# Performance work log

Measured on AMD Instinct MI355X. Metric: run time of the kernel, lower is better.

## Reference

```python
import jax, jax.numpy as jnp
import numpy as np

B, N, D, H = 4, 1024, 256, 8  # batch, seq, in_dim(=per-head qkv_dim), n_heads


def setup_inputs() -> dict:
    key = jax.random.key(0)
    k1, k2, k3 = jax.random.split(key, 3)
    x = jax.random.normal(k1, (B, N, D), dtype=jnp.float32)
    Wqkv = jax.random.normal(k2, (D, 3 * D * H), dtype=jnp.float32) * 0.02
    bqkv = jnp.zeros((3 * D * H,), dtype=jnp.float32)
    W0 = jax.random.normal(k3, (D * H, D), dtype=jnp.float32) * 0.02
    b0 = jnp.zeros((D,), dtype=jnp.float32)
    return {"x": x, "Wqkv": Wqkv, "bqkv": bqkv, "W0": W0, "b0": b0}


def reference(x, Wqkv, bqkv, W0, b0):
    b, n, d = x.shape
    h = Wqkv.shape[1] // (3 * d)
    qkv = x @ Wqkv + bqkv                      # [b, n, 3*d*h]
    # Faithful to torch: raw row-major reinterpretation of the buffer.
    q, k, v = jnp.reshape(qkv, (3, b, n, d, h))
    score = jnp.einsum('bnqh,btqh->bnth', q, k) * (d ** -0.5)  # [b, n, n, h]
    attn = jax.nn.softmax(score, axis=1)       # softmax over query axis (dim=1), as in source
    # einsum 'bnnh,bnqh->bnqh' = diagonal of attn times v (faithful to source)
    av = jnp.einsum('bnnh,bnqh->bnqh', attn, v)  # [b, n, d, h]
    out = av.reshape(b, n, d * h) @ W0 + b0    # [b, n, d]
    return out
```

## Files before the change

### kernel.cpp

```cpp
#include <hip/hip_runtime.h>


#define SEGSZ 8388608

typedef short v8s __attribute__((ext_vector_type(8)));
typedef float v4f __attribute__((ext_vector_type(4)));

__device__ __forceinline__ ushort f2bf(float v) {
  union { float f; unsigned u; } x; x.f = v;
  const unsigned r = x.u + 0x7fff + ((x.u >> 16) & 1);
  return (ushort)(r >> 16);
}
__device__ __forceinline__ float bf2f(ushort v) {
  union { unsigned u; float f; } x; x.u = ((unsigned)v) << 16;
  return x.f;
}

#define GLOAD_LDS16(g, l)                                            \
  __builtin_amdgcn_global_load_lds(                                  \
      (const __attribute__((address_space(1))) void*)(g),            \
      (__attribute__((address_space(3))) void*)(l), 16, 0, 0)

__global__ __launch_bounds__(256) void prep(
    const float* __restrict__ X, const float* __restrict__ Wqkv,
    const float* __restrict__ W0, ushort* __restrict__ xb,
    ushort* __restrict__ whT, ushort* __restrict__ w0T) {
  __shared__ float T[64][65];
  const int tid = threadIdx.x;
  int bid = blockIdx.x;

  if (bid < 1024) {
    const size_t i = ((size_t)bid * 256 + tid) * 4;
    const float4 v = *(const float4*)&X[i];
    ushort4 hv = {f2bf(v.x), f2bf(v.y), f2bf(v.z), f2bf(v.w)};
    *(ushort4*)&xb[i] = hv;
    return;
  }
  bid -= 1024;
  if (bid < 384) {
    const int n0 = (bid % 96) * 64;
    const int k0 = (bid / 96) * 64;
    {
      const int row = tid >> 2;
      const int c0 = (tid & 3) * 16;
#pragma unroll
      for (int j = 0; j < 16; j += 4) {
        const float4 v = *(const float4*)&Wqkv[(size_t)(k0 + row) * 6144 + n0 + c0 + j];
        T[row][c0 + j + 0] = v.x; T[row][c0 + j + 1] = v.y;
        T[row][c0 + j + 2] = v.z; T[row][c0 + j + 3] = v.w;
      }
    }
    __syncthreads();
    {
      const int nn = tid >> 2;
      const int kk0 = (tid & 3) * 16;
      const int n = n0 + nn;
      const int seg = n >> 11, h = n & 7, d = (n & 2047) >> 3;
      const int p = seg * 2048 + h * 256 + d;
      ushort hv[16];
#pragma unroll
      for (int j = 0; j < 16; ++j) hv[j] = f2bf(T[kk0 + j][nn]);
      const size_t base = (size_t)p * 256 + k0 + kk0;
#pragma unroll
      for (int j = 0; j < 16; j += 8) *(v8s*)&whT[base + j] = *(v8s*)&hv[j];
    }
    return;
  }
  bid -= 384;
  {
    const int e0 = (bid & 3) * 64;
    const int k0 = (bid >> 2) * 64;
    {
      const int row = tid >> 2;
      const int c0 = (tid & 3) * 16;
#pragma unroll
      for (int j = 0; j < 16; j += 4) {
        const float4 v = *(const float4*)&W0[(size_t)(k0 + row) * 256 + e0 + c0 + j];
        T[row][c0 + j + 0] = v.x; T[row][c0 + j + 1] = v.y;
        T[row][c0 + j + 2] = v.z; T[row][c0 + j + 3] = v.w;
      }
    }
    __syncthreads();
    {
      const int ee = tid >> 2;
      const int kk0 = (tid & 3) * 16;
#pragma unroll
      for (int j = 0; j < 16; ++j) {
        const int k = k0 + kk0 + j;
        const int d = k >> 3, h = k & 7;
        w0T[(size_t)(e0 + ee) * 2048 + h * 256 + d] = f2bf(T[kk0 + j][ee]);
      }
    }
  }
}

__global__ __launch_bounds__(256) void qkv_mfma(
    const ushort* __restrict__ xb, const ushort* __restrict__ whT,
    const float* __restrict__ bias, ushort* __restrict__ qkvb) {
  __shared__ ushort As[128 * 32];
  __shared__ ushort Bh[128 * 32];
  const int tid = threadIdx.x;
  const int wave = tid >> 6, lane = tid & 63;
  const int quad = lane >> 4, l15 = lane & 15;
  const int c0 = blockIdx.x * 128;
  const int r0 = blockIdx.y * 128;
  const int wr = (wave >> 1) * 64;
  const int wc = (wave & 1) * 64;

  v4f acc[4][4] = {};

  for (int d0 = 0; d0 < 256; d0 += 32) {
#pragma unroll
    for (int half = 0; half < 2; ++half) {
      const int rr = wave * 32 + half * 16;
      const int row = rr + (lane >> 2);
      const int gcol = d0 + (lane & 3) * 8;
      GLOAD_LDS16(xb + (size_t)(r0 + row) * 256 + gcol, &As[rr * 32]);
      GLOAD_LDS16(whT + (size_t)(c0 + row) * 256 + gcol, &Bh[rr * 32]);
    }
    __syncthreads();

    v8s aF[4], bF[4];
#pragma unroll
    for (int i = 0; i < 4; ++i) {
      aF[i] = *(const v8s*)&As[(wr + i * 16 + l15) * 32 + quad * 8];
      bF[i] = *(const v8s*)&Bh[(wc + i * 16 + l15) * 32 + quad * 8];
    }
#pragma unroll
    for (int ri = 0; ri < 4; ++ri)
#pragma unroll
      for (int ci = 0; ci < 4; ++ci)
        acc[ri][ci] = __builtin_amdgcn_mfma_f32_16x16x32_bf16(
            aF[ri], bF[ci], acc[ri][ci], 0, 0, 0);
    __syncthreads();
  }

#pragma unroll
  for (int ci = 0; ci < 4; ++ci) {
    const int c = c0 + wc + ci * 16 + l15;
    const int cseg = c >> 11;
    const int h = (c & 2047) >> 8;
    const int d = c & 255;
    const float bv = bias[cseg * 2048 + d * 8 + h];
#pragma unroll
    for (int ri = 0; ri < 4; ++ri)
#pragma unroll
      for (int rg = 0; rg < 4; ++rg) {
        const int r = r0 + wr + ri * 16 + quad * 4 + rg;
        const int g = r * 3 + cseg;
        const int seg = g >> 12;
        const int tok = g & 4095;
        float val = acc[ri][ci][rg] + bv;
        if (seg == 0) val *= 0.0625f;
        qkvb[(size_t)seg * SEGSZ + (size_t)tok * 2048 + h * 256 + d] = f2bf(val);
      }
  }
}

__global__ __launch_bounds__(256) void mid_fused(
    const ushort* __restrict__ qkvb, const ushort* __restrict__ w0T,
    float* __restrict__ pl, float* __restrict__ sd_ws,
    ushort* __restrict__ partial) {
  __shared__ ushort S1[128 * 32];
  __shared__ ushort S2[128 * 32];
  __shared__ float redL[2][2][64];

  const int tid = threadIdx.x;
  const int wave = tid >> 6, lane = tid & 63;
  const int quad = lane >> 4, l15 = lane & 15;
  const int wr = (wave >> 1) * 64;
  const int wc = (wave & 1) * 64;
  const int id = blockIdx.x;

  v4f acc[4][4] = {};

  if (id < 2048) {
    const int bh = (id >> 9) * 8 + (id & 7);
    const int tile = (id >> 3) & 63;
    const int tt0 = (tile >> 3) * 128;
    const int nn0 = (tile & 7) * 128;
    const int b = bh >> 3, h = bh & 7;
    const ushort* Qg = qkvb + (size_t)b * 1024 * 2048 + h * 256;
    const ushort* Kg = Qg + SEGSZ;

    for (int d0 = 0; d0 < 256; d0 += 32) {
#pragma unroll
      for (int half = 0; half < 2; ++half) {
        const int rr = wave * 32 + half * 16;
        const int row = rr + (lane >> 2);
        const int gcol = d0 + (lane & 3) * 8;
        GLOAD_LDS16(Qg + (size_t)(nn0 + row) * 2048 + gcol, &S1[rr * 32]);
        GLOAD_LDS16(Kg + (size_t)(tt0 + row) * 2048 + gcol, &S2[rr * 32]);
      }
      __syncthreads();

      v8s aF[4], bF[4];
#pragma unroll
      for (int i = 0; i < 4; ++i) {
        aF[i] = *(const v8s*)&S1[(wr + i * 16 + l15) * 32 + quad * 8];
        bF[i] = *(const v8s*)&S2[(wc + i * 16 + l15) * 32 + quad * 8];
      }
#pragma unroll
      for (int ri = 0; ri < 4; ++ri)
#pragma unroll
        for (int ci = 0; ci < 4; ++ci)
          acc[ri][ci] = __builtin_amdgcn_mfma_f32_16x16x32_bf16(
              aF[ri], bF[ci], acc[ri][ci], 0, 0, 0);
      __syncthreads();
    }

    float lsum[4];
#pragma unroll
    for (int ci = 0; ci < 4; ++ci) {
      float s = 0.f;
#pragma unroll
      for (int ri = 0; ri < 4; ++ri)
#pragma unroll
        for (int rg = 0; rg < 4; ++rg) s += __expf(acc[ri][ci][rg]);
      s += __shfl_xor(s, 16, 64);
      s += __shfl_xor(s, 32, 64);
      lsum[ci] = s;
    }
    if (quad == 0) {
#pragma unroll
      for (int ci = 0; ci < 4; ++ci)
        redL[wave & 1][wave >> 1][ci * 16 + l15] = lsum[ci];
    }
    __syncthreads();
    if ((wave >> 1) == 0 && quad == 0) {
#pragma unroll
      for (int ci = 0; ci < 4; ++ci) {
        const int t = tt0 + (wave & 1) * 64 + ci * 16 + l15;
        const float l = lsum[ci] + redL[wave & 1][1][ci * 16 + l15];
        pl[((size_t)bh * 1024 + t) * 8 + (tile & 7)] = l;
      }
    }

    if (tt0 == nn0 && (wave == 0 || wave == 3) && quad == (l15 >> 2)) {
#pragma unroll
      for (int ri = 0; ri < 4; ++ri) {
        const int t = tt0 + (wave & 1) * 64 + ri * 16 + l15;
        sd_ws[(size_t)bh * 1024 + t] = acc[ri][ri][l15 & 3];
      }
    }
  } else {
    const int j = id - 2048;
    const int e0 = (j & 1) * 128;
    const int tok0 = ((j >> 1) & 31) * 128;
    const int h = j >> 6;
    const int kbase = h * 256;
    const ushort* vb = qkvb + 2 * (size_t)SEGSZ;

    for (int d0 = 0; d0 < 256; d0 += 32) {
#pragma unroll
      for (int half = 0; half < 2; ++half) {
        const int rr = wave * 32 + half * 16;
        const int row = rr + (lane >> 2);
        const int gcol = kbase + d0 + (lane & 3) * 8;
        GLOAD_LDS16(vb + (size_t)(tok0 + row) * 2048 + gcol, &S1[rr * 32]);
        GLOAD_LDS16(w0T + (size_t)(e0 + row) * 2048 + gcol, &S2[rr * 32]);
      }
      __syncthreads();

      v8s aF[4], bF[4];
#pragma unroll
      for (int i = 0; i < 4; ++i) {
        aF[i] = *(const v8s*)&S1[(wr + i * 16 + l15) * 32 + quad * 8];
        bF[i] = *(const v8s*)&S2[(wc + i * 16 + l15) * 32 + quad * 8];
      }
#pragma unroll
      for (int ri = 0; ri < 4; ++ri)
#pragma unroll
        for (int ci = 0; ci < 4; ++ci)
          acc[ri][ci] = __builtin_amdgcn_mfma_f32_16x16x32_bf16(
              aF[ri], bF[ci], acc[ri][ci], 0, 0, 0);
      __syncthreads();
    }

#pragma unroll
    for (int ri = 0; ri < 4; ++ri)
#pragma unroll
      for (int rg = 0; rg < 4; ++rg) {
        const int lrow = wr + ri * 16 + quad * 4 + rg;
        const int tok = tok0 + lrow;
#pragma unroll
        for (int ci = 0; ci < 4; ++ci) {
          const int e = e0 + wc + ci * 16 + l15;
          partial[(size_t)h * 1048576 + (size_t)tok * 256 + e] =
              f2bf(acc[ri][ci][rg]);
        }
      }
  }
}

__global__ __launch_bounds__(256) void av_atomic(
    const ushort* __restrict__ vb, const ushort* __restrict__ w0T,
    const float* __restrict__ pl, const float* __restrict__ sd,
    float* __restrict__ out) {
  __shared__ ushort As[128 * 32];
  __shared__ ushort Bs[128 * 32];
  __shared__ float diagS[128];
  const int tid = threadIdx.x;
  const int wave = tid >> 6, lane = tid & 63;
  const int quad = lane >> 4, l15 = lane & 15;
  const int e0 = blockIdx.x * 128;
  const int tok0 = blockIdx.y * 128;
  const int h = blockIdx.z;
  const int kbase = h * 256;
  const int wr = (wave >> 1) * 64;
  const int wc = (wave & 1) * 64;

  if (tid < 128) {
    const int bh = (tok0 >> 10) * 8 + h;
    const int t = (tok0 & 1023) + tid;
    const size_t base = ((size_t)bh * 1024 + t) * 8;
    float l = 0.f;
#pragma unroll
    for (int c = 0; c < 8; ++c) l += pl[base + c];
    diagS[tid] = __expf(sd[(size_t)bh * 1024 + t]) / l;
  }

  v4f acc[4][4] = {};

  for (int d0 = 0; d0 < 256; d0 += 32) {
#pragma unroll
    for (int half = 0; half < 2; ++half) {
      const int rr = wave * 32 + half * 16;
      const int row = rr + (lane >> 2);
      const int gcol = kbase + d0 + (lane & 3) * 8;
      GLOAD_LDS16(vb + (size_t)(tok0 + row) * 2048 + gcol, &As[rr * 32]);
      GLOAD_LDS16(w0T + (size_t)(e0 + row) * 2048 + gcol, &Bs[rr * 32]);
    }
    __syncthreads();

    v8s aF[4], bF[4];
#pragma unroll
    for (int i = 0; i < 4; ++i) {
      aF[i] = *(const v8s*)&As[(wr + i * 16 + l15) * 32 + quad * 8];
      bF[i] = *(const v8s*)&Bs[(wc + i * 16 + l15) * 32 + quad * 8];
    }
#pragma unroll
    for (int ri = 0; ri < 4; ++ri)
#pragma unroll
      for (int ci = 0; ci < 4; ++ci)
        acc[ri][ci] =
            __builtin_amdgcn_mfma_f32_16x16x32_bf16(aF[ri], bF[ci], acc[ri][ci], 0, 0, 0);
    __syncthreads();
  }

#pragma unroll
  for (int ri = 0; ri < 4; ++ri)
#pragma unroll
    for (int rg = 0; rg < 4; ++rg) {
      const int lrow = wr + ri * 16 + quad * 4 + rg;
      const int tok = tok0 + lrow;
      const float dg = diagS[lrow];
#pragma unroll
      for (int ci = 0; ci < 4; ++ci) {
        const int e = e0 + wc + ci * 16 + l15;
        atomicAdd(&out[(size_t)tok * 256 + e], acc[ri][ci][rg] * dg);
      }
    }
}

__global__ void init_out(const float* __restrict__ b0, float* __restrict__ out) {
  const int i = blockIdx.x * 256 + threadIdx.x;
  const int e0 = (i & 63) << 2;
  *(float4*)&out[(size_t)i * 4] = *(const float4*)&b0[e0];
}

__global__ void reduce_out(const ushort* __restrict__ partial,
                           const float* __restrict__ pl,
                           const float* __restrict__ sd,
                           const float* __restrict__ b0, float* __restrict__ out) {
  __shared__ float dgS[32];
  const int i = blockIdx.x * 256 + threadIdx.x;
  const int tbase = blockIdx.x * 4;
  if (threadIdx.x < 32) {
    const int tl = threadIdx.x >> 3, h = threadIdx.x & 7;
    const int tok = tbase + tl;
    const int bh = (tok >> 10) * 8 + h;
    const int t = tok & 1023;
    const size_t base = ((size_t)bh * 1024 + t) * 8;
    float l = 0.f;
#pragma unroll
    for (int c = 0; c < 8; ++c) l += pl[base + c];
    dgS[threadIdx.x] = __expf(sd[(size_t)bh * 1024 + t]) / l;
  }
  __syncthreads();
  const int tl = threadIdx.x >> 6;
  const int e0 = (i & 63) << 2;
  float4 a = *(const float4*)&b0[e0];
#pragma unroll
  for (int h = 0; h < 8; ++h) {
    const float dg = dgS[tl * 8 + h];
    const ushort4 p = *(const ushort4*)&partial[(size_t)h * 1048576 + (size_t)i * 4];
    a.x += dg * bf2f(p.x); a.y += dg * bf2f(p.y);
    a.z += dg * bf2f(p.z); a.w += dg * bf2f(p.w);
  }
  *(float4*)&out[(size_t)i * 4] = a;
}

extern "C" void kernel_launch(void* const* d_in, const int* in_sizes, int n_in,
                              void* d_out, int out_size, void* d_ws, size_t ws_size,
                              hipStream_t stream) {
  const float* x    = (const float*)d_in[0];
  const float* Wqkv = (const float*)d_in[1];
  const float* bqkv = (const float*)d_in[2];
  const float* W0   = (const float*)d_in[3];
  const float* b0   = (const float*)d_in[4];
  float* out = (float*)d_out;

  float*  pl   = (float*)d_ws;
  float*  sd   = pl + 262144;
  ushort* qkvb = (ushort*)(sd + 32768);
  ushort* xb   = qkvb + 3 * (size_t)SEGSZ;
  ushort* whT  = xb + 1048576;
  ushort* w0T  = whT + 1572864;
  ushort* partial = w0T + 524288;

  ushort* vb = qkvb + 2 * (size_t)SEGSZ;

  const size_t need_base =
      (size_t)(262144 + 32768) * 4 + (size_t)SEGSZ * 3 * 2 +
      (size_t)(1048576 + 1572864 + 524288) * 2;
  const bool full = ws_size >= need_base + (size_t)8 * 1048576 * 2;

  prep<<<1536, 256, 0, stream>>>(x, Wqkv, W0, xb, whT, w0T);
  qkv_mfma<<<dim3(48, 32), 256, 0, stream>>>(xb, whT, bqkv, qkvb);
  if (full) {
    mid_fused<<<2560, 256, 0, stream>>>(qkvb, w0T, pl, sd, partial);
    reduce_out<<<1024, 256, 0, stream>>>(partial, pl, sd, b0, out);
  } else {
    scores_fallback:
    mid_fused<<<2048, 256, 0, stream>>>(qkvb, w0T, pl, sd, nullptr);
    init_out<<<1024, 256, 0, stream>>>(b0, out);
    av_atomic<<<dim3(2, 32, 8), 256, 0, stream>>>(vb, w0T, pl, sd, out);
  }
}
```

Baseline: 135.2 us.

## Use 256x256 double-buffered 8-wave GEMM tiles for QKV and mid kernels

Replaces the 128x128, 4-wave, single-buffered MFMA GEMMs with a shared 256x256, 8-wave routine. It double-buffers K-tiles of 64 in LDS with an XOR swizzle, and interleaves async global-to-LDS loads with MFMA phases using explicit vmcnt waits, barriers and setprio. The goal is more operand reuse per tile, hidden load latency and fewer LDS bank conflicts. Costs are larger LDS use (128KB per block), fewer blocks in the grid, and a partial-sum layout for pl that shrinks from 8 to 4 slots per token.

```diff
diff --git a/kernel.cpp b/kernel.cpp
--- a/kernel.cpp
+++ b/kernel.cpp
@@ -20,6 +20,10 @@
   __builtin_amdgcn_global_load_lds(                                  \
       (const __attribute__((address_space(1))) void*)(g),            \
       (__attribute__((address_space(3))) void*)(l), 16, 0, 0)
+
+#define SBAR()   asm volatile("s_barrier" ::: "memory")
+#define VMCNT4() asm volatile("s_waitcnt vmcnt(4)" ::: "memory")
+#define VMCNT0() asm volatile("s_waitcnt vmcnt(0)" ::: "memory")
 
 __global__ __launch_bounds__(256) void prep(
     const float* __restrict__ X, const float* __restrict__ Wqkv,
@@ -94,202 +98,219 @@
   }
 }
 
-__global__ __launch_bounds__(256) void qkv_mfma(
+template <int STRIDE>
+__device__ __forceinline__ void gemm256_8ph(
+    const ushort* __restrict__ gA, const ushort* __restrict__ gB,
+    ushort (&AS)[2][16384], ushort (&BS)[2][16384],
+    v4f (&acc)[2][2][4][2]) {
+  const int tid = threadIdx.x;
+  const int wave = tid >> 6, lane = tid & 63;
+  const int wm = wave >> 2, wn = wave & 3;
+  const int quad = lane >> 4, l15 = lane & 15;
+  const int srow = wave * 8 + (lane >> 3);
+  const int scol = ((lane & 7) << 3) ^ (((lane >> 5) & 1) << 4);
+  const int cq = (quad * 8) ^ (((l15 >> 2) & 1) << 4);
+
+  auto stage = [&](int op, int buf, int half, int kt) {
+#pragma unroll
+    for (int j = 0; j < 2; ++j) {
+      const size_t grow =
+          (size_t)(half * 128 + j * 64 + srow) * STRIDE + kt * 64 + scol;
+      ushort* lb = op ? &BS[buf][half * 8192 + j * 4096 + wave * 512]
+                      : &AS[buf][half * 8192 + j * 4096 + wave * 512];
+      GLOAD_LDS16((op ? gB : gA) + grow, lb);
+    }
+  };
+
+  stage(0, 0, 0, 0); stage(0, 0, 1, 0); stage(1, 0, 0, 0); stage(1, 0, 1, 0);
+  stage(0, 1, 0, 1); stage(1, 1, 0, 1);
+  VMCNT4();
+  SBAR();
+
+  for (int it = 0; it < 2; ++it) {
+    const int t0 = it * 2;
+#pragma unroll
+    for (int p = 0; p < 8; ++p) {
+      const int kb = p >> 2;
+      const int qr = (p >> 1) & 1, qc = p & 1;
+      v8s af[4][2], bfr[2][2];
+#pragma unroll
+      for (int ri = 0; ri < 4; ++ri) {
+        const int r = qr * 128 + wm * 64 + ri * 16 + l15;
+#pragma unroll
+        for (int ks = 0; ks < 2; ++ks)
+          af[ri][ks] = *(const v8s*)&AS[kb][r * 64 + ks * 32 + cq];
+      }
+#pragma unroll
+      for (int ci = 0; ci < 2; ++ci) {
+        const int r = qc * 128 + wn * 32 + ci * 16 + l15;
+#pragma unroll
+        for (int ks = 0; ks < 2; ++ks)
+          bfr[ci][ks] = *(const v8s*)&BS[kb][r * 64 + ks * 32 + cq];
+      }
+      {
+        const int st = t0 + 1 + ((p + 2) >> 2);
+        if (st < 4) stage(p & 1, st & 1, 1 - ((p >> 1) & 1), st);
+      }
+      SBAR();
+      __builtin_amdgcn_s_setprio(1);
+#pragma unroll
+      for (int ri = 0; ri < 4; ++ri)
+#pragma unroll
+        for (int ci = 0; ci < 2; ++ci)
+#pragma unroll
+          for (int ks = 0; ks < 2; ++ks)
+            acc[qr][qc][ri][ci] = __builtin_amdgcn_mfma_f32_16x16x32_bf16(
+                af[ri][ks], bfr[ci][ks], acc[qr][qc][ri][ci], 0, 0, 0);
+      __builtin_amdgcn_s_setprio(0);
+      if (p == 3 || p == 7) { if (it == 0) VMCNT4(); else VMCNT0(); }
+      SBAR();
+    }
+  }
+}
+
+__global__ __launch_bounds__(512, 2) void qkv8(
     const ushort* __restrict__ xb, const ushort* __restrict__ whT,
     const float* __restrict__ bias, ushort* __restrict__ qkvb) {
-  __shared__ ushort As[128 * 32];
-  __shared__ ushort Bh[128 * 32];
+  __shared__ ushort AS[2][16384];
+  __shared__ ushort BS[2][16384];
   const int tid = threadIdx.x;
   const int wave = tid >> 6, lane = tid & 63;
+  const int wm = wave >> 2, wn = wave & 3;
   const int quad = lane >> 4, l15 = lane & 15;
-  const int c0 = blockIdx.x * 128;
-  const int r0 = blockIdx.y * 128;
-  const int wr = (wave >> 1) * 64;
-  const int wc = (wave & 1) * 64;
-
-  v4f acc[4][4] = {};
-
-  for (int d0 = 0; d0 < 256; d0 += 32) {
-#pragma unroll
-    for (int half = 0; half < 2; ++half) {
-      const int rr = wave * 32 + half * 16;
-      const int row = rr + (lane >> 2);
-      const int gcol = d0 + (lane & 3) * 8;
-      GLOAD_LDS16(xb + (size_t)(r0 + row) * 256 + gcol, &As[rr * 32]);
-      GLOAD_LDS16(whT + (size_t)(c0 + row) * 256 + gcol, &Bh[rr * 32]);
-    }
-    __syncthreads();
-
-    v8s aF[4], bF[4];
-#pragma unroll
-    for (int i = 0; i < 4; ++i) {
-      aF[i] = *(const v8s*)&As[(wr + i * 16 + l15) * 32 + quad * 8];
-      bF[i] = *(const v8s*)&Bh[(wc + i * 16 + l15) * 32 + quad * 8];
-    }
-#pragma unroll
-    for (int ri = 0; ri < 4; ++ri)
-#pragma unroll
-      for (int ci = 0; ci < 4; ++ci)
-        acc[ri][ci] = __builtin_amdgcn_mfma_f32_16x16x32_bf16(
-            aF[ri], bF[ci], acc[ri][ci], 0, 0, 0);
-    __syncthreads();
-  }
-
-#pragma unroll
-  for (int ci = 0; ci < 4; ++ci) {
-    const int c = c0 + wc + ci * 16 + l15;
-    const int cseg = c >> 11;
-    const int h = (c & 2047) >> 8;
-    const int d = c & 255;
-    const float bv = bias[cseg * 2048 + d * 8 + h];
-#pragma unroll
-    for (int ri = 0; ri < 4; ++ri)
-#pragma unroll
-      for (int rg = 0; rg < 4; ++rg) {
-        const int r = r0 + wr + ri * 16 + quad * 4 + rg;
-        const int g = r * 3 + cseg;
-        const int seg = g >> 12;
-        const int tok = g & 4095;
-        float val = acc[ri][ci][rg] + bv;
-        if (seg == 0) val *= 0.0625f;
-        qkvb[(size_t)seg * SEGSZ + (size_t)tok * 2048 + h * 256 + d] = f2bf(val);
-      }
-  }
-}
-
-__global__ __launch_bounds__(256) void mid_fused(
+  const int c0 = blockIdx.x * 256;
+  const int r0 = blockIdx.y * 256;
+
+  v4f acc[2][2][4][2] = {};
+  gemm256_8ph<256>(xb + (size_t)r0 * 256, whT + (size_t)c0 * 256, AS, BS, acc);
+
+#pragma unroll
+  for (int qc2 = 0; qc2 < 2; ++qc2)
+#pragma unroll
+    for (int ci = 0; ci < 2; ++ci) {
+      const int cc = c0 + qc2 * 128 + wn * 32 + ci * 16 + l15;
+      const int cseg = cc >> 11;
+      const int hh = (cc & 2047) >> 8;
+      const int d = cc & 255;
+      const float bv = bias[cseg * 2048 + d * 8 + hh];
+#pragma unroll
+      for (int qr = 0; qr < 2; ++qr)
+#pragma unroll
+        for (int ri = 0; ri < 4; ++ri)
+#pragma unroll
+          for (int rg = 0; rg < 4; ++rg) {
+            const int r = r0 + qr * 128 + wm * 64 + ri * 16 + quad * 4 + rg;
+            const int g = r * 3 + cseg;
+            const int seg = g >> 12;
+            const int tok = g & 4095;
+            float val = acc[qr][qc2][ri][ci][rg] + bv;
+            if (seg == 0) val *= 0.0625f;
+            qkvb[(size_t)seg * SEGSZ + (size_t)tok * 2048 + hh * 256 + d] = f2bf(val);
+          }
+    }
+}
+
+__global__ __launch_bounds__(512, 2) void mid8(
     const ushort* __restrict__ qkvb, const ushort* __restrict__ w0T,
     float* __restrict__ pl, float* __restrict__ sd_ws,
     ushort* __restrict__ partial) {
-  __shared__ ushort S1[128 * 32];
-  __shared__ ushort S2[128 * 32];
-  __shared__ float redL[2][2][64];
-
+  __shared__ ushort AS[2][16384];
+  __shared__ ushort BS[2][16384];
+  __shared__ float redL[2][4][64];
   const int tid = threadIdx.x;
   const int wave = tid >> 6, lane = tid & 63;
+  const int wm = wave >> 2, wn = wave & 3;
   const int quad = lane >> 4, l15 = lane & 15;
-  const int wr = (wave >> 1) * 64;
-  const int wc = (wave & 1) * 64;
   const int id = blockIdx.x;
 
-  v4f acc[4][4] = {};
-
-  if (id < 2048) {
-    const int bh = (id >> 9) * 8 + (id & 7);
-    const int tile = (id >> 3) & 63;
-    const int tt0 = (tile >> 3) * 128;
-    const int nn0 = (tile & 7) * 128;
+  v4f acc[2][2][4][2] = {};
+
+  if (id < 512) {
+    const int c = id & 7, inner = id >> 3;
+    const int bh = (inner >> 4) * 8 + c;
+    const int tile = inner & 15;
+    const int tt0 = (tile >> 2) * 256;
+    const int nn0 = (tile & 3) * 256;
     const int b = bh >> 3, h = bh & 7;
-    const ushort* Qg = qkvb + (size_t)b * 1024 * 2048 + h * 256;
-    const ushort* Kg = Qg + SEGSZ;
-
-    for (int d0 = 0; d0 < 256; d0 += 32) {
-#pragma unroll
-      for (int half = 0; half < 2; ++half) {
-        const int rr = wave * 32 + half * 16;
-        const int row = rr + (lane >> 2);
-        const int gcol = d0 + (lane & 3) * 8;
-        GLOAD_LDS16(Qg + (size_t)(nn0 + row) * 2048 + gcol, &S1[rr * 32]);
-        GLOAD_LDS16(Kg + (size_t)(tt0 + row) * 2048 + gcol, &S2[rr * 32]);
-      }
-      __syncthreads();
-
-      v8s aF[4], bF[4];
-#pragma unroll
-      for (int i = 0; i < 4; ++i) {
-        aF[i] = *(const v8s*)&S1[(wr + i * 16 + l15) * 32 + quad * 8];
-        bF[i] = *(const v8s*)&S2[(wc + i * 16 + l15) * 32 + quad * 8];
-      }
+    const ushort* Qg = qkvb + (size_t)b * 2097152 + h * 256 + (size_t)nn0 * 2048;
+    const ushort* Kg = qkvb + SEGSZ + (size_t)b * 2097152 + h * 256 + (size_t)tt0 * 2048;
+    gemm256_8ph<2048>(Qg, Kg, AS, BS, acc);
+
+    float lsum[2][2];
+#pragma unroll
+    for (int qc2 = 0; qc2 < 2; ++qc2)
+#pragma unroll
+      for (int ci = 0; ci < 2; ++ci) {
+        float s = 0.f;
+#pragma unroll
+        for (int qr = 0; qr < 2; ++qr)
+#pragma unroll
+          for (int ri = 0; ri < 4; ++ri)
+#pragma unroll
+            for (int rg = 0; rg < 4; ++rg)
+              s += __expf(acc[qr][qc2][ri][ci][rg]);
+        s += __shfl_xor(s, 16, 64);
+        s += __shfl_xor(s, 32, 64);
+        lsum[qc2][ci] = s;
+      }
+    if (quad == 0) {
+#pragma unroll
+      for (int qc2 = 0; qc2 < 2; ++qc2)
+#pragma unroll
+        for (int ci = 0; ci < 2; ++ci)
+          redL[wm][wn][(qc2 * 2 + ci) * 16 + l15] = lsum[qc2][ci];
+    }
+    __syncthreads();
+    if (wm == 0 && quad == 0) {
+#pragma unroll
+      for (int qc2 = 0; qc2 < 2; ++qc2)
+#pragma unroll
+        for (int ci = 0; ci < 2; ++ci) {
+          const int t = tt0 + qc2 * 128 + wn * 32 + ci * 16 + l15;
+          const float l = lsum[qc2][ci] + redL[1][wn][(qc2 * 2 + ci) * 16 + l15];
+          pl[((size_t)bh * 1024 + t) * 4 + (nn0 >> 8)] = l;
+        }
+    }
+
+    if (tt0 == nn0) {
+#pragma unroll
+      for (int qr = 0; qr < 2; ++qr)
+#pragma unroll
+        for (int ci = 0; ci < 2; ++ci)
+#pragma unroll
+          for (int ri = 0; ri < 4; ++ri)
+#pragma unroll
+            for (int rg = 0; rg < 4; ++rg)
+              if (wn * 2 + ci - wm * 4 == ri && (l15 >> 2) == quad &&
+                  (l15 & 3) == rg) {
+                const int t = tt0 + qr * 128 + wm * 64 + ri * 16 + l15;
+                sd_ws[(size_t)bh * 1024 + t] = acc[qr][qr][ri][ci][rg];
+              }
+    }
+  } else {
+    const int j = id - 512;
+    const int h = j >> 4;
+    const int tok0 = (j & 15) * 256;
+    const ushort* Ag = qkvb + 2 * (size_t)SEGSZ + (size_t)tok0 * 2048 + h * 256;
+    const ushort* Bg = w0T + h * 256;
+    gemm256_8ph<2048>(Ag, Bg, AS, BS, acc);
+
+#pragma unroll
+    for (int qr = 0; qr < 2; ++qr)
 #pragma unroll
       for (int ri = 0; ri < 4; ++ri)
 #pragma unroll
-        for (int ci = 0; ci < 4; ++ci)
-          acc[ri][ci] = __builtin_amdgcn_mfma_f32_16x16x32_bf16(
-              aF[ri], bF[ci], acc[ri][ci], 0, 0, 0);
-      __syncthreads();
-    }
-
-    float lsum[4];
-#pragma unroll
-    for (int ci = 0; ci < 4; ++ci) {
-      float s = 0.f;
-#pragma unroll
-      for (int ri = 0; ri < 4; ++ri)
-#pragma unroll
-        for (int rg = 0; rg < 4; ++rg) s += __expf(acc[ri][ci][rg]);
-      s += __shfl_xor(s, 16, 64);
-      s += __shfl_xor(s, 32, 64);
-      lsum[ci] = s;
-    }
-    if (quad == 0) {
-#pragma unroll
-      for (int ci = 0; ci < 4; ++ci)
-        redL[wave & 1][wave >> 1][ci * 16 + l15] = lsum[ci];
-    }
-    __syncthreads();
-    if ((wave >> 1) == 0 && quad == 0) {
-#pragma unroll
-      for (int ci = 0; ci < 4; ++ci) {
-        const int t = tt0 + (wave & 1) * 64 + ci * 16 + l15;
-        const float l = lsum[ci] + redL[wave & 1][1][ci * 16 + l15];
-        pl[((size_t)bh * 1024 + t) * 8 + (tile & 7)] = l;
-      }
-    }
-
-    if (tt0 == nn0 && (wave == 0 || wave == 3) && quad == (l15 >> 2)) {
-#pragma unroll
-      for (int ri = 0; ri < 4; ++ri) {
-        const int t = tt0 + (wave & 1) * 64 + ri * 16 + l15;
-        sd_ws[(size_t)bh * 1024 + t] = acc[ri][ri][l15 & 3];
-      }
-    }
-  } else {
-    const int j = id - 2048;
-    const int e0 = (j & 1) * 128;
-    const int tok0 = ((j >> 1) & 31) * 128;
-    const int h = j >> 6;
-    const int kbase = h * 256;
-    const ushort* vb = qkvb + 2 * (size_t)SEGSZ;
-
-    for (int d0 = 0; d0 < 256; d0 += 32) {
-#pragma unroll
-      for (int half = 0; half < 2; ++half) {
-        const int rr = wave * 32 + half * 16;
-        const int row = rr + (lane >> 2);
-        const int gcol = kbase + d0 + (lane & 3) * 8;
-        GLOAD_LDS16(vb + (size_t)(tok0 + row) * 2048 + gcol, &S1[rr * 32]);
-        GLOAD_LDS16(w0T + (size_t)(e0 + row) * 2048 + gcol, &S2[rr * 32]);
-      }
-      __syncthreads();
-
-      v8s aF[4], bF[4];
-#pragma unroll
-      for (int i = 0; i < 4; ++i) {
-        aF[i] = *(const v8s*)&S1[(wr + i * 16 + l15) * 32 + quad * 8];
-        bF[i] = *(const v8s*)&S2[(wc + i * 16 + l15) * 32 + quad * 8];
-      }
-#pragma unroll
-      for (int ri = 0; ri < 4; ++ri)
-#pragma unroll
-        for (int ci = 0; ci < 4; ++ci)
-          acc[ri][ci] = __builtin_amdgcn_mfma_f32_16x16x32_bf16(
-              aF[ri], bF[ci], acc[ri][ci], 0, 0, 0);
-      __syncthreads();
-    }
-
-#pragma unroll
-    for (int ri = 0; ri < 4; ++ri)
-#pragma unroll
-      for (int rg = 0; rg < 4; ++rg) {
-        const int lrow = wr + ri * 16 + quad * 4 + rg;
-        const int tok = tok0 + lrow;
-#pragma unroll
-        for (int ci = 0; ci < 4; ++ci) {
-          const int e = e0 + wc + ci * 16 + l15;
-          partial[(size_t)h * 1048576 + (size_t)tok * 256 + e] =
-              f2bf(acc[ri][ci][rg]);
+        for (int rg = 0; rg < 4; ++rg) {
+          const int tok = tok0 + qr * 128 + wm * 64 + ri * 16 + quad * 4 + rg;
+#pragma unroll
+          for (int qc2 = 0; qc2 < 2; ++qc2)
+#pragma unroll
+            for (int ci = 0; ci < 2; ++ci) {
+              const int e = qc2 * 128 + wn * 32 + ci * 16 + l15;
+              partial[(size_t)h * 1048576 + (size_t)tok * 256 + e] =
+                  f2bf(acc[qr][qc2][ri][ci][rg]);
+            }
         }
-      }
   }
 }
 
@@ -313,10 +334,10 @@
   if (tid < 128) {
     const int bh = (tok0 >> 10) * 8 + h;
     const int t = (tok0 & 1023) + tid;
-    const size_t base = ((size_t)bh * 1024 + t) * 8;
+    const size_t base = ((size_t)bh * 1024 + t) * 4;
     float l = 0.f;
 #pragma unroll
-    for (int c = 0; c < 8; ++c) l += pl[base + c];
+    for (int cc = 0; cc < 4; ++cc) l += pl[base + cc];
     diagS[tid] = __expf(sd[(size_t)bh * 1024 + t]) / l;
   }
 
@@ -381,10 +402,10 @@
     const int tok = tbase + tl;
     const int bh = (tok >> 10) * 8 + h;
     const int t = tok & 1023;
-    const size_t base = ((size_t)bh * 1024 + t) * 8;
+    const size_t base = ((size_t)bh * 1024 + t) * 4;
     float l = 0.f;
 #pragma unroll
-    for (int c = 0; c < 8; ++c) l += pl[base + c];
+    for (int cc = 0; cc < 4; ++cc) l += pl[base + cc];
     dgS[threadIdx.x] = __expf(sd[(size_t)bh * 1024 + t]) / l;
   }
   __syncthreads();
@@ -427,13 +448,12 @@
   const bool full = ws_size >= need_base + (size_t)8 * 1048576 * 2;
 
   prep<<<1536, 256, 0, stream>>>(x, Wqkv, W0, xb, whT, w0T);
-  qkv_mfma<<<dim3(48, 32), 256, 0, stream>>>(xb, whT, bqkv, qkvb);
+  qkv8<<<dim3(24, 16), 512, 0, stream>>>(xb, whT, bqkv, qkvb);
   if (full) {
-    mid_fused<<<2560, 256, 0, stream>>>(qkvb, w0T, pl, sd, partial);
+    mid8<<<640, 512, 0, stream>>>(qkvb, w0T, pl, sd, partial);
     reduce_out<<<1024, 256, 0, stream>>>(partial, pl, sd, b0, out);
   } else {
-    scores_fallback:
-    mid_fused<<<2048, 256, 0, stream>>>(qkvb, w0T, pl, sd, nullptr);
+    mid8<<<512, 512, 0, stream>>>(qkvb, w0T, pl, sd, nullptr);
     init_out<<<1024, 256, 0, stream>>>(b0, out);
     av_atomic<<<dim3(2, 32, 8), 256, 0, stream>>>(vb, w0T, pl, sd, out);
   }
```

New measurement: 151.8 us. 1.12x slower.

## Double-buffer LDS tiles in QKV, score and AV-projection GEMM loops

Applied to the files above, without the earlier changes.

Each of the three MFMA GEMM loops now uses two LDS buffers. The global-to-LDS loads for the next K-slice are issued before the MFMAs on the current slice, so there is one barrier per iteration instead of two. The intent is to hide global load latency behind matrix math. In exchange, shared memory per block roughly doubles, which may lower occupancy. An extra barrier is added before the reduction scratch reuse, and an unused label is removed.

```diff
diff --git a/kernel.cpp b/kernel.cpp
--- a/kernel.cpp
+++ b/kernel.cpp
@@ -97,8 +97,8 @@
 __global__ __launch_bounds__(256) void qkv_mfma(
     const ushort* __restrict__ xb, const ushort* __restrict__ whT,
     const float* __restrict__ bias, ushort* __restrict__ qkvb) {
-  __shared__ ushort As[128 * 32];
-  __shared__ ushort Bh[128 * 32];
+  __shared__ ushort As[2][128 * 32];
+  __shared__ ushort Bh[2][128 * 32];
   const int tid = threadIdx.x;
   const int wave = tid >> 6, lane = tid & 63;
   const int quad = lane >> 4, l15 = lane & 15;
@@ -107,24 +107,30 @@
   const int wr = (wave >> 1) * 64;
   const int wc = (wave & 1) * 64;
 
-  v4f acc[4][4] = {};
-
-  for (int d0 = 0; d0 < 256; d0 += 32) {
+  auto stage = [&](int d0, int bi) {
 #pragma unroll
     for (int half = 0; half < 2; ++half) {
       const int rr = wave * 32 + half * 16;
       const int row = rr + (lane >> 2);
       const int gcol = d0 + (lane & 3) * 8;
-      GLOAD_LDS16(xb + (size_t)(r0 + row) * 256 + gcol, &As[rr * 32]);
-      GLOAD_LDS16(whT + (size_t)(c0 + row) * 256 + gcol, &Bh[rr * 32]);
-    }
-    __syncthreads();
-
+      GLOAD_LDS16(xb + (size_t)(r0 + row) * 256 + gcol, &As[bi][rr * 32]);
+      GLOAD_LDS16(whT + (size_t)(c0 + row) * 256 + gcol, &Bh[bi][rr * 32]);
+    }
+  };
+
+  v4f acc[4][4] = {};
+
+  stage(0, 0);
+  __syncthreads();
+#pragma unroll
+  for (int kt = 0; kt < 8; ++kt) {
+    const int cur = kt & 1;
+    if (kt < 7) stage((kt + 1) * 32, cur ^ 1);
     v8s aF[4], bF[4];
 #pragma unroll
     for (int i = 0; i < 4; ++i) {
-      aF[i] = *(const v8s*)&As[(wr + i * 16 + l15) * 32 + quad * 8];
-      bF[i] = *(const v8s*)&Bh[(wc + i * 16 + l15) * 32 + quad * 8];
+      aF[i] = *(const v8s*)&As[cur][(wr + i * 16 + l15) * 32 + quad * 8];
+      bF[i] = *(const v8s*)&Bh[cur][(wc + i * 16 + l15) * 32 + quad * 8];
     }
 #pragma unroll
     for (int ri = 0; ri < 4; ++ri)
@@ -132,7 +138,7 @@
       for (int ci = 0; ci < 4; ++ci)
         acc[ri][ci] = __builtin_amdgcn_mfma_f32_16x16x32_bf16(
             aF[ri], bF[ci], acc[ri][ci], 0, 0, 0);
-    __syncthreads();
+    if (kt < 7) __syncthreads();
   }
 
 #pragma unroll
@@ -161,8 +167,8 @@
     const ushort* __restrict__ qkvb, const ushort* __restrict__ w0T,
     float* __restrict__ pl, float* __restrict__ sd_ws,
     ushort* __restrict__ partial) {
-  __shared__ ushort S1[128 * 32];
-  __shared__ ushort S2[128 * 32];
+  __shared__ ushort S1[2][128 * 32];
+  __shared__ ushort S2[2][128 * 32];
   __shared__ float redL[2][2][64];
 
   const int tid = threadIdx.x;
@@ -183,22 +189,28 @@
     const ushort* Qg = qkvb + (size_t)b * 1024 * 2048 + h * 256;
     const ushort* Kg = Qg + SEGSZ;
 
-    for (int d0 = 0; d0 < 256; d0 += 32) {
+    auto stage = [&](int d0, int bi) {
 #pragma unroll
       for (int half = 0; half < 2; ++half) {
         const int rr = wave * 32 + half * 16;
         const int row = rr + (lane >> 2);
         const int gcol = d0 + (lane & 3) * 8;
-        GLOAD_LDS16(Qg + (size_t)(nn0 + row) * 2048 + gcol, &S1[rr * 32]);
-        GLOAD_LDS16(Kg + (size_t)(tt0 + row) * 2048 + gcol, &S2[rr * 32]);
-      }
-      __syncthreads();
-
+        GLOAD_LDS16(Qg + (size_t)(nn0 + row) * 2048 + gcol, &S1[bi][rr * 32]);
+        GLOAD_LDS16(Kg + (size_t)(tt0 + row) * 2048 + gcol, &S2[bi][rr * 32]);
+      }
+    };
+
+    stage(0, 0);
+    __syncthreads();
+#pragma unroll
+    for (int kt = 0; kt < 8; ++kt) {
+      const int cur = kt & 1;
+      if (kt < 7) stage((kt + 1) * 32, cur ^ 1);
       v8s aF[4], bF[4];
 #pragma unroll
       for (int i = 0; i < 4; ++i) {
-        aF[i] = *(const v8s*)&S1[(wr + i * 16 + l15) * 32 + quad * 8];
-        bF[i] = *(const v8s*)&S2[(wc + i * 16 + l15) * 32 + quad * 8];
+        aF[i] = *(const v8s*)&S1[cur][(wr + i * 16 + l15) * 32 + quad * 8];
+        bF[i] = *(const v8s*)&S2[cur][(wc + i * 16 + l15) * 32 + quad * 8];
       }
 #pragma unroll
       for (int ri = 0; ri < 4; ++ri)
@@ -206,7 +218,7 @@
         for (int ci = 0; ci < 4; ++ci)
           acc[ri][ci] = __builtin_amdgcn_mfma_f32_16x16x32_bf16(
               aF[ri], bF[ci], acc[ri][ci], 0, 0, 0);
-      __syncthreads();
+      if (kt < 7) __syncthreads();
     }
 
     float lsum[4];
@@ -221,6 +233,7 @@
       s += __shfl_xor(s, 32, 64);
       lsum[ci] = s;
     }
+    __syncthreads();
     if (quad == 0) {
 #pragma unroll
       for (int ci = 0; ci < 4; ++ci)
@@ -251,22 +264,28 @@
     const int kbase = h * 256;
     const ushort* vb = qkvb + 2 * (size_t)SEGSZ;
 
-    for (int d0 = 0; d0 < 256; d0 += 32) {
+    auto stage = [&](int d0, int bi) {
 #pragma unroll
       for (int half = 0; half < 2; ++half) {
         const int rr = wave * 32 + half * 16;
         const int row = rr + (lane >> 2);
         const int gcol = kbase + d0 + (lane & 3) * 8;
-        GLOAD_LDS16(vb + (size_t)(tok0 + row) * 2048 + gcol, &S1[rr * 32]);
-        GLOAD_LDS16(w0T + (size_t)(e0 + row) * 2048 + gcol, &S2[rr * 32]);
-      }
-      __syncthreads();
-
+        GLOAD_LDS16(vb + (size_t)(tok0 + row) * 2048 + gcol, &S1[bi][rr * 32]);
+        GLOAD_LDS16(w0T + (size_t)(e0 + row) * 2048 + gcol, &S2[bi][rr * 32]);
+      }
+    };
+
+    stage(0, 0);
+    __syncthreads();
+#pragma unroll
+    for (int kt = 0; kt < 8; ++kt) {
+      const int cur = kt & 1;
+      if (kt < 7) stage((kt + 1) * 32, cur ^ 1);
       v8s aF[4], bF[4];
 #pragma unroll
       for (int i = 0; i < 4; ++i) {
-        aF[i] = *(const v8s*)&S1[(wr + i * 16 + l15) * 32 + quad * 8];
-        bF[i] = *(const v8s*)&S2[(wc + i * 16 + l15) * 32 + quad * 8];
+        aF[i] = *(const v8s*)&S1[cur][(wr + i * 16 + l15) * 32 + quad * 8];
+        bF[i] = *(const v8s*)&S2[cur][(wc + i * 16 + l15) * 32 + quad * 8];
       }
 #pragma unroll
       for (int ri = 0; ri < 4; ++ri)
@@ -274,7 +293,7 @@
         for (int ci = 0; ci < 4; ++ci)
           acc[ri][ci] = __builtin_amdgcn_mfma_f32_16x16x32_bf16(
               aF[ri], bF[ci], acc[ri][ci], 0, 0, 0);
-      __syncthreads();
+      if (kt < 7) __syncthreads();
     }
 
 #pragma unroll
@@ -432,7 +451,6 @@
     mid_fused<<<2560, 256, 0, stream>>>(qkvb, w0T, pl, sd, partial);
     reduce_out<<<1024, 256, 0, stream>>>(partial, pl, sd, b0, out);
   } else {
-    scores_fallback:
     mid_fused<<<2048, 256, 0, stream>>>(qkvb, w0T, pl, sd, nullptr);
     init_out<<<1024, 256, 0, stream>>>(b0, out);
     av_atomic<<<dim3(2, 32, 8), 256, 0, stream>>>(vb, w0T, pl, sd, out);
```

Measured after the change: 137.0 us. About the same (+1.4%).

## Share a K=64 XOR-swizzled LDS GEMM tile helper across all bf16 GEMMs

Applied to the files above, without the earlier changes.

Replaces the per-kernel K=32 GEMM main loops with one shared helper that stages K=64 slices (doubling the LDS tiles) and XOR-swizzles the LDS column layout. The goal is to halve the number of barrier pairs per K sweep and cut LDS bank conflicts on the fragment reads. The cost is twice the LDS per block, which may reduce occupancy. It also adds a missing sync after the diagS fill in the atomic fallback path.

```diff
diff --git a/kernel.cpp b/kernel.cpp
--- a/kernel.cpp
+++ b/kernel.cpp
@@ -94,11 +94,55 @@
   }
 }
 
+template <int STRIDE>
+__device__ __forceinline__ void gemm128_k64(
+    const ushort* __restrict__ gA, const ushort* __restrict__ gB,
+    ushort (&AS)[8192], ushort (&BS)[8192], v4f (&acc)[4][4]) {
+  const int tid = threadIdx.x;
+  const int wave = tid >> 6, lane = tid & 63;
+  const int quad = lane >> 4, l15 = lane & 15;
+  const int wr = (wave >> 1) * 64;
+  const int wc = (wave & 1) * 64;
+  const int srow = lane >> 3;
+  const int scol = (((lane & 7) ^ srow) << 3);
+
+#pragma unroll
+  for (int kt = 0; kt < 4; ++kt) {
+#pragma unroll
+    for (int j = 0; j < 4; ++j) {
+      const size_t grow =
+          (size_t)(j * 32 + wave * 8 + srow) * STRIDE + kt * 64 + scol;
+      GLOAD_LDS16(gA + grow, &AS[j * 2048 + wave * 512]);
+      GLOAD_LDS16(gB + grow, &BS[j * 2048 + wave * 512]);
+    }
+    __syncthreads();
+#pragma unroll
+    for (int ks = 0; ks < 2; ++ks) {
+      v8s aF[4], bF[4];
+      const int rx = l15 & 7;
+#pragma unroll
+      for (int i = 0; i < 4; ++i) {
+        aF[i] = *(const v8s*)&AS[(wr + i * 16 + l15) * 64 +
+                                 ((((ks << 2) | quad) ^ rx) << 3)];
+        bF[i] = *(const v8s*)&BS[(wc + i * 16 + l15) * 64 +
+                                 ((((ks << 2) | quad) ^ rx) << 3)];
+      }
+#pragma unroll
+      for (int ri = 0; ri < 4; ++ri)
+#pragma unroll
+        for (int ci = 0; ci < 4; ++ci)
+          acc[ri][ci] = __builtin_amdgcn_mfma_f32_16x16x32_bf16(
+              aF[ri], bF[ci], acc[ri][ci], 0, 0, 0);
+    }
+    __syncthreads();
+  }
+}
+
 __global__ __launch_bounds__(256) void qkv_mfma(
     const ushort* __restrict__ xb, const ushort* __restrict__ whT,
     const float* __restrict__ bias, ushort* __restrict__ qkvb) {
-  __shared__ ushort As[128 * 32];
-  __shared__ ushort Bh[128 * 32];
+  __shared__ ushort As[8192];
+  __shared__ ushort Bh[8192];
   const int tid = threadIdx.x;
   const int wave = tid >> 6, lane = tid & 63;
   const int quad = lane >> 4, l15 = lane & 15;
@@ -108,32 +152,7 @@
   const int wc = (wave & 1) * 64;
 
   v4f acc[4][4] = {};
-
-  for (int d0 = 0; d0 < 256; d0 += 32) {
-#pragma unroll
-    for (int half = 0; half < 2; ++half) {
-      const int rr = wave * 32 + half * 16;
-      const int row = rr + (lane >> 2);
-      const int gcol = d0 + (lane & 3) * 8;
-      GLOAD_LDS16(xb + (size_t)(r0 + row) * 256 + gcol, &As[rr * 32]);
-      GLOAD_LDS16(whT + (size_t)(c0 + row) * 256 + gcol, &Bh[rr * 32]);
-    }
-    __syncthreads();
-
-    v8s aF[4], bF[4];
-#pragma unroll
-    for (int i = 0; i < 4; ++i) {
-      aF[i] = *(const v8s*)&As[(wr + i * 16 + l15) * 32 + quad * 8];
-      bF[i] = *(const v8s*)&Bh[(wc + i * 16 + l15) * 32 + quad * 8];
-    }
-#pragma unroll
-    for (int ri = 0; ri < 4; ++ri)
-#pragma unroll
-      for (int ci = 0; ci < 4; ++ci)
-        acc[ri][ci] = __builtin_amdgcn_mfma_f32_16x16x32_bf16(
-            aF[ri], bF[ci], acc[ri][ci], 0, 0, 0);
-    __syncthreads();
-  }
+  gemm128_k64<256>(xb + (size_t)r0 * 256, whT + (size_t)c0 * 256, As, Bh, acc);
 
 #pragma unroll
   for (int ci = 0; ci < 4; ++ci) {
@@ -161,8 +180,8 @@
     const ushort* __restrict__ qkvb, const ushort* __restrict__ w0T,
     float* __restrict__ pl, float* __restrict__ sd_ws,
     ushort* __restrict__ partial) {
-  __shared__ ushort S1[128 * 32];
-  __shared__ ushort S2[128 * 32];
+  __shared__ ushort S1[8192];
+  __shared__ ushort S2[8192];
   __shared__ float redL[2][2][64];
 
   const int tid = threadIdx.x;
@@ -183,31 +202,8 @@
     const ushort* Qg = qkvb + (size_t)b * 1024 * 2048 + h * 256;
     const ushort* Kg = Qg + SEGSZ;
 
-    for (int d0 = 0; d0 < 256; d0 += 32) {
-#pragma unroll
-      for (int half = 0; half < 2; ++half) {
-        const int rr = wave * 32 + half * 16;
-        const int row = rr + (lane >> 2);
-        const int gcol = d0 + (lane & 3) * 8;
-        GLOAD_LDS16(Qg + (size_t)(nn0 + row) * 2048 + gcol, &S1[rr * 32]);
-        GLOAD_LDS16(Kg + (size_t)(tt0 + row) * 2048 + gcol, &S2[rr * 32]);
-      }
-      __syncthreads();
-
-      v8s aF[4], bF[4];
-#pragma unroll
-      for (int i = 0; i < 4; ++i) {
-        aF[i] = *(const v8s*)&S1[(wr + i * 16 + l15) * 32 + quad * 8];
-        bF[i] = *(const v8s*)&S2[(wc + i * 16 + l15) * 32 + quad * 8];
-      }
-#pragma unroll
-      for (int ri = 0; ri < 4; ++ri)
-#pragma unroll
-        for (int ci = 0; ci < 4; ++ci)
-          acc[ri][ci] = __builtin_amdgcn_mfma_f32_16x16x32_bf16(
-              aF[ri], bF[ci], acc[ri][ci], 0, 0, 0);
-      __syncthreads();
-    }
+    gemm128_k64<2048>(Qg + (size_t)nn0 * 2048, Kg + (size_t)tt0 * 2048,
+                      S1, S2, acc);
 
     float lsum[4];
 #pragma unroll
@@ -248,34 +244,10 @@
     const int e0 = (j & 1) * 128;
     const int tok0 = ((j >> 1) & 31) * 128;
     const int h = j >> 6;
-    const int kbase = h * 256;
     const ushort* vb = qkvb + 2 * (size_t)SEGSZ;
 
-    for (int d0 = 0; d0 < 256; d0 += 32) {
-#pragma unroll
-      for (int half = 0; half < 2; ++half) {
-        const int rr = wave * 32 + half * 16;
-        const int row = rr + (lane >> 2);
-        const int gcol = kbase + d0 + (lane & 3) * 8;
-        GLOAD_LDS16(vb + (size_t)(tok0 + row) * 2048 + gcol, &S1[rr * 32]);
-        GLOAD_LDS16(w0T + (size_t)(e0 + row) * 2048 + gcol, &S2[rr * 32]);
-      }
-      __syncthreads();
-
-      v8s aF[4], bF[4];
-#pragma unroll
-      for (int i = 0; i < 4; ++i) {
-        aF[i] = *(const v8s*)&S1[(wr + i * 16 + l15) * 32 + quad * 8];
-        bF[i] = *(const v8s*)&S2[(wc + i * 16 + l15) * 32 + quad * 8];
-      }
-#pragma unroll
-      for (int ri = 0; ri < 4; ++ri)
-#pragma unroll
-        for (int ci = 0; ci < 4; ++ci)
-          acc[ri][ci] = __builtin_amdgcn_mfma_f32_16x16x32_bf16(
-              aF[ri], bF[ci], acc[ri][ci], 0, 0, 0);
-      __syncthreads();
-    }
+    gemm128_k64<2048>(vb + (size_t)tok0 * 2048 + h * 256,
+                      w0T + (size_t)e0 * 2048 + h * 256, S1, S2, acc);
 
 #pragma unroll
     for (int ri = 0; ri < 4; ++ri)
@@ -297,8 +269,8 @@
     const ushort* __restrict__ vb, const ushort* __restrict__ w0T,
     const float* __restrict__ pl, const float* __restrict__ sd,
     float* __restrict__ out) {
-  __shared__ ushort As[128 * 32];
-  __shared__ ushort Bs[128 * 32];
+  __shared__ ushort As[8192];
+  __shared__ ushort Bs[8192];
   __shared__ float diagS[128];
   const int tid = threadIdx.x;
   const int wave = tid >> 6, lane = tid & 63;
@@ -306,7 +278,6 @@
   const int e0 = blockIdx.x * 128;
   const int tok0 = blockIdx.y * 128;
   const int h = blockIdx.z;
-  const int kbase = h * 256;
   const int wr = (wave >> 1) * 64;
   const int wc = (wave & 1) * 64;
 
@@ -319,34 +290,11 @@
     for (int c = 0; c < 8; ++c) l += pl[base + c];
     diagS[tid] = __expf(sd[(size_t)bh * 1024 + t]) / l;
   }
+  __syncthreads();
 
   v4f acc[4][4] = {};
-
-  for (int d0 = 0; d0 < 256; d0 += 32) {
-#pragma unroll
-    for (int half = 0; half < 2; ++half) {
-      const int rr = wave * 32 + half * 16;
-      const int row = rr + (lane >> 2);
-      const int gcol = kbase + d0 + (lane & 3) * 8;
-      GLOAD_LDS16(vb + (size_t)(tok0 + row) * 2048 + gcol, &As[rr * 32]);
-      GLOAD_LDS16(w0T + (size_t)(e0 + row) * 2048 + gcol, &Bs[rr * 32]);
-    }
-    __syncthreads();
-
-    v8s aF[4], bF[4];
-#pragma unroll
-    for (int i = 0; i < 4; ++i) {
-      aF[i] = *(const v8s*)&As[(wr + i * 16 + l15) * 32 + quad * 8];
-      bF[i] = *(const v8s*)&Bs[(wc + i * 16 + l15) * 32 + quad * 8];
-    }
-#pragma unroll
-    for (int ri = 0; ri < 4; ++ri)
-#pragma unroll
-      for (int ci = 0; ci < 4; ++ci)
-        acc[ri][ci] =
-            __builtin_amdgcn_mfma_f32_16x16x32_bf16(aF[ri], bF[ci], acc[ri][ci], 0, 0, 0);
-    __syncthreads();
-  }
+  gemm128_k64<2048>(vb + (size_t)tok0 * 2048 + h * 256,
+                    w0T + (size_t)e0 * 2048 + h * 256, As, Bs, acc);
 
 #pragma unroll
   for (int ri = 0; ri < 4; ++ri)
@@ -432,7 +380,6 @@
     mid_fused<<<2560, 256, 0, stream>>>(qkvb, w0T, pl, sd, partial);
     reduce_out<<<1024, 256, 0, stream>>>(partial, pl, sd, b0, out);
   } else {
-    scores_fallback:
     mid_fused<<<2048, 256, 0, stream>>>(qkvb, w0T, pl, sd, nullptr);
     init_out<<<1024, 256, 0, stream>>>(b0, out);
     av_atomic<<<dim3(2, 32, 8), 256, 0, stream>>>(vb, w0T, pl, sd, out);
```

Measured after the change: 127.5 us (median of 2 runs). 5.7% less time.
